# Kernel optimization log

Hardware: AMD Instinct MI355X
Metric: run time of the kernel (lower is better)

Reference implementation:

```python
import jax, jax.numpy as jnp
import numpy as np

N = 10000      # nodes
E = 320000     # edges (avg degree 32)
D_IN = 128
D_H = 256
D_C = 32       # comm_dim
D_OUT = 64


def setup_inputs() -> dict:
    key = jax.random.key(0)
    ks = jax.random.split(key, 14)
    p = lambda k, shape: jax.random.normal(k, shape, jnp.float32) * 0.02
    return {
        "x": jax.random.normal(ks[0], (N, D_IN), jnp.float32),
        "edge_index": jax.random.randint(ks[1], (2, E), 0, N),
        "W_in": p(ks[2], (D_IN, D_H)), "b_in": jnp.zeros((D_H,), jnp.float32),
        "Wq": p(ks[3], (D_H, D_C)),   "bq": jnp.zeros((D_C,), jnp.float32),
        "Wk": p(ks[4], (D_H, D_C)),   "bk": jnp.zeros((D_C,), jnp.float32),
        "Wv": p(ks[5], (D_H, D_H)),   "bv": jnp.zeros((D_H,), jnp.float32),
        "W1": p(ks[6], (2 * D_H, D_H)), "b1": jnp.zeros((D_H,), jnp.float32),
        "W2": p(ks[7], (D_H, D_OUT)),  "b2": jnp.zeros((D_OUT,), jnp.float32),
    }


def reference(x, edge_index, W_in, b_in, Wq, bq, Wk, bk, Wv, bv, W1, b1, W2, b2):
    n = x.shape[0]
    h = x @ W_in + b_in                       # [N, D_H]
    q = h @ Wq + bq                           # [N, D_C]
    k = h @ Wk + bk                           # [N, D_C]
    v = h @ Wv + bv                           # [N, D_H]
    scores = (q @ k.T) / np.sqrt(q.shape[-1]).astype(np.float32)  # [N, N]
    # torch: zeros -> scatter 1 at edges -> masked_fill(==0, -inf);
    # edge positions keep value 1.0 ADDED to scores (faithful quirk).
    mask = jnp.full((n, n), -jnp.inf, jnp.float32)
    mask = mask.at[edge_index[0], edge_index[1]].set(1.0)
    w = jax.nn.softmax(scores + mask, axis=-1)
    w = jnp.nan_to_num(w, nan=0.0)            # rows with no edges -> all zeros
    comm = w @ v                              # [N, D_H]
    combined = jnp.concatenate([h, comm], axis=-1)  # [N, 2*D_H]
    return jax.nn.relu(combined @ W1 + b1) @ W2 + b2  # [N, D_OUT]
```

## Files before the change

### kernel.cpp

```cpp
#include <hip/hip_runtime.h>
#include <stdint.h>
#include <stddef.h>

constexpr int N_NODES = 10000;
constexpr int N_EDGES = 320000;
constexpr int DIM_IN  = 128;
constexpr int DIM_H   = 256;
constexpr int DIM_C   = 32;
constexpr int DIM_OUT = 64;
constexpr int DIM_QKV = DIM_C + DIM_C + DIM_H;
constexpr int DIM_QK  = 2 * DIM_C;
constexpr int DIM_CAT = 2 * DIM_H;
constexpr float SCALE = 0.17677669529663687f;
constexpr int MAXD = 192;
constexpr float VSCALE = 64.0f;

#if __has_builtin(__builtin_amdgcn_cvt_pk_f32_fp8) && __has_builtin(__builtin_amdgcn_cvt_pk_fp8_f32)
#define V_FP8 1
#else
#define V_FP8 0
#endif

constexpr size_t alignw(size_t w) { return (w + 15) & ~size_t(15); }
constexpr size_t OFF_DEG    = 0;
constexpr size_t OFF_COL    = alignw(OFF_DEG + N_NODES);
constexpr size_t OFF_QK     = alignw(OFF_COL + (size_t)N_NODES * MAXD);
constexpr size_t OFF_BQKV   = alignw(OFF_QK + (size_t)N_NODES * DIM_QK);
constexpr size_t OFF_VBF    = alignw(OFF_BQKV + DIM_QKV);
constexpr size_t OFF_XBF    = alignw(OFF_VBF + (size_t)N_NODES * DIM_H / 2);
constexpr size_t OFF_CATBF  = alignw(OFF_XBF + (size_t)N_NODES * DIM_IN / 2);
constexpr size_t OFF_WINT   = alignw(OFF_CATBF + (size_t)N_NODES * DIM_CAT / 2);
constexpr size_t OFF_WQKVT  = alignw(OFF_WINT + (size_t)DIM_H * DIM_IN / 2);
constexpr size_t OFF_W1T    = alignw(OFF_WQKVT + (size_t)DIM_QKV * DIM_H / 2);
constexpr size_t OFF_W2T    = alignw(OFF_W1T + (size_t)DIM_H * DIM_CAT / 2);

typedef __attribute__((ext_vector_type(8))) short short8;
typedef __attribute__((ext_vector_type(4))) float floatx4;
typedef __attribute__((ext_vector_type(2))) float floatx2;

__device__ inline unsigned short f2bf(float f) {
    uint32_t u = __builtin_bit_cast(uint32_t, f);
    uint32_t r = (u + 0x7fffu + ((u >> 16) & 1u)) >> 16;
    return (unsigned short)r;
}
__device__ inline float bf2f_lo(uint32_t u) { return __builtin_bit_cast(float, u << 16); }
__device__ inline float bf2f_hi(uint32_t u) { return __builtin_bit_cast(float, u & 0xffff0000u); }

template <bool RELU, int MODE>
__global__ __launch_bounds__(256)
void mfma_gemm(const unsigned short* __restrict__ A, int lda,
               const unsigned short* __restrict__ Bt,
               const float* __restrict__ bias,
               float* __restrict__ Cf, unsigned short* __restrict__ Cb, int ldc,
               int M, int K)
{
    constexpr int BM = 128, BN = 64, PAD = 40;
    __shared__ short As[BM * PAD];
    __shared__ short Bs[BN * PAD];
    const int tid   = threadIdx.x;
    const int wave  = tid >> 6;
    const int lane  = tid & 63;
    const int quad  = lane >> 4;
    const int col16 = lane & 15;
    const int row0  = blockIdx.y * BM;
    const int col0  = blockIdx.x * BN;

    floatx4 acc[2][4] = {};

    const int sr = tid >> 2;
    const int sc = (tid & 3) * 8;

    for (int k0 = 0; k0 < K; k0 += 32) {
        #pragma unroll
        for (int i = 0; i < 2; ++i) {
            int r = sr + i * 64;
            int gr = row0 + r;
            short8 v = {};
            if (gr < M) v = *(const short8*)(A + (size_t)gr * lda + k0 + sc);
            *(short8*)(As + r * PAD + sc) = v;
        }
        {
            short8 v = *(const short8*)(Bt + (size_t)(col0 + sr) * K + k0 + sc);
            *(short8*)(Bs + sr * PAD + sc) = v;
        }
        __syncthreads();
        short8 a0 = *(const short8*)(As + (wave * 32 + col16) * PAD + quad * 8);
        short8 a1 = *(const short8*)(As + (wave * 32 + 16 + col16) * PAD + quad * 8);
        #pragma unroll
        for (int nf = 0; nf < 4; ++nf) {
            short8 b = *(const short8*)(Bs + (nf * 16 + col16) * PAD + quad * 8);
            acc[0][nf] = __builtin_amdgcn_mfma_f32_16x16x32_bf16(a0, b, acc[0][nf], 0, 0, 0);
            acc[1][nf] = __builtin_amdgcn_mfma_f32_16x16x32_bf16(a1, b, acc[1][nf], 0, 0, 0);
        }
        __syncthreads();
    }
    #pragma unroll
    for (int mf = 0; mf < 2; ++mf)
        #pragma unroll
        for (int r = 0; r < 4; ++r) {
            int gr = row0 + wave * 32 + mf * 16 + quad * 4 + r;
            if (gr >= M) continue;
            #pragma unroll
            for (int nf = 0; nf < 4; ++nf) {
                int gc = col0 + nf * 16 + col16;
                float v = acc[mf][nf][r] + bias[gc];
                if (RELU) v = fmaxf(v, 0.f);
                if (MODE == 2) {
                    if (gc < DIM_QK) {
                        Cf[(size_t)gr * DIM_QK + gc] = v;
                    } else {
#if V_FP8
                        int pk = __builtin_amdgcn_cvt_pk_fp8_f32(v * VSCALE, 0.f, 0, false);
                        ((unsigned char*)Cb)[(size_t)gr * DIM_H + (gc - DIM_QK)] =
                            (unsigned char)(pk & 0xff);
#else
                        Cb[(size_t)gr * DIM_H + (gc - DIM_QK)] = f2bf(v);
#endif
                    }
                } else {
                    Cb[(size_t)gr * ldc + gc] = f2bf(v);
                }
            }
        }
}

__global__ __launch_bounds__(256)
void gemm_w1w2(const unsigned short* __restrict__ cat, const unsigned short* __restrict__ W1T,
               const float* __restrict__ b1, const unsigned short* __restrict__ W2T,
               const float* __restrict__ b2, float* __restrict__ out, int M)
{
    constexpr int PAD = 40, TP = 260;
    __shared__ short As[64 * PAD];
    __shared__ short BsTs[64 * TP];
    short* Bs = BsTs;
    short* Ts = BsTs;
    const int tid   = threadIdx.x;
    const int wave  = tid >> 6;
    const int lane  = tid & 63;
    const int quad  = lane >> 4;
    const int col16 = lane & 15;
    const int row0  = blockIdx.x * 64;

    const int sr = tid >> 2;
    const int sc = (tid & 3) * 8;

    floatx4 acc[16] = {};
    for (int k0 = 0; k0 < DIM_CAT; k0 += 32) {
        {
            int gr = row0 + sr;
            short8 v = {};
            if (gr < M) v = *(const short8*)(cat + (size_t)gr * DIM_CAT + k0 + sc);
            *(short8*)(As + sr * PAD + sc) = v;
        }
        #pragma unroll
        for (int p = 0; p < 4; ++p) {
            int r = sr + p * 64;
            *(short8*)(Bs + r * PAD + sc) = *(const short8*)(W1T + (size_t)r * DIM_CAT + k0 + sc);
        }
        __syncthreads();
        short8 a = *(const short8*)(As + (wave * 16 + col16) * PAD + quad * 8);
        #pragma unroll
        for (int nf = 0; nf < 16; ++nf) {
            short8 b = *(const short8*)(Bs + (nf * 16 + col16) * PAD + quad * 8);
            acc[nf] = __builtin_amdgcn_mfma_f32_16x16x32_bf16(a, b, acc[nf], 0, 0, 0);
        }
        __syncthreads();
    }

    #pragma unroll
    for (int nf = 0; nf < 16; ++nf) {
        int gc = nf * 16 + col16;
        float bia = b1[gc];
        #pragma unroll
        for (int r = 0; r < 4; ++r) {
            int lr = wave * 16 + quad * 4 + r;
            float v = fmaxf(acc[nf][r] + bia, 0.f);
            Ts[lr * TP + gc] = (short)f2bf(v);
        }
    }
    __syncthreads();

    floatx4 acc2[4] = {};
    for (int k0 = 0; k0 < DIM_H; k0 += 32) {
        short8 a = *(const short8*)(Ts + (wave * 16 + col16) * TP + k0 + quad * 8);
        #pragma unroll
        for (int nf = 0; nf < 4; ++nf) {
            int brow = nf * 16 + col16;
            short8 b = *(const short8*)(W2T + (size_t)brow * DIM_H + k0 + quad * 8);
            acc2[nf] = __builtin_amdgcn_mfma_f32_16x16x32_bf16(a, b, acc2[nf], 0, 0, 0);
        }
    }
    #pragma unroll
    for (int nf = 0; nf < 4; ++nf) {
        int gc = nf * 16 + col16;
        float bia = b2[gc];
        #pragma unroll
        for (int r = 0; r < 4; ++r) {
            int gr = row0 + wave * 16 + quad * 4 + r;
            if (gr < M) out[(size_t)gr * DIM_OUT + gc] = acc2[nf][r] + bia;
        }
    }
}

__global__ void zero_deg(int* __restrict__ deg) {
    int i = blockIdx.x * blockDim.x + threadIdx.x;
    if (i < N_NODES) deg[i] = 0;
}

__global__ void prep_all(const float* __restrict__ x, const int* __restrict__ ei,
                         const float* __restrict__ W_in,
                         const float* __restrict__ Wq, const float* __restrict__ Wk,
                         const float* __restrict__ Wv,
                         const float* __restrict__ bq, const float* __restrict__ bk,
                         const float* __restrict__ bv,
                         const float* __restrict__ W1, const float* __restrict__ W2,
                         int* __restrict__ deg, int* __restrict__ col,
                         unsigned short* __restrict__ xb,
                         unsigned short* __restrict__ WinT, unsigned short* __restrict__ WqkvT,
                         unsigned short* __restrict__ W1T, unsigned short* __restrict__ W2T,
                         float* __restrict__ bqkv)
{
    int i = blockIdx.x * blockDim.x + threadIdx.x;
    int stride = gridDim.x * blockDim.x;
    for (int e = i; e < N_EDGES; e += stride) {
        int src = ei[e];
        int dst = ei[N_EDGES + e];
        int slot = atomicAdd(&deg[src], 1);
        if (slot < MAXD) col[src * MAXD + slot] = dst;
    }
    for (int idx = i; idx < (N_NODES * DIM_IN) / 8; idx += stride) {
        float4 a = ((const float4*)x)[2 * idx];
        float4 b = ((const float4*)x)[2 * idx + 1];
        uint4 o;
        o.x = (uint32_t)f2bf(a.x) | ((uint32_t)f2bf(a.y) << 16);
        o.y = (uint32_t)f2bf(a.z) | ((uint32_t)f2bf(a.w) << 16);
        o.z = (uint32_t)f2bf(b.x) | ((uint32_t)f2bf(b.y) << 16);
        o.w = (uint32_t)f2bf(b.z) | ((uint32_t)f2bf(b.w) << 16);
        ((uint4*)xb)[idx] = o;
    }
    for (int idx = i; idx < DIM_H * DIM_IN; idx += stride) {
        int n = idx / DIM_IN, k = idx % DIM_IN;
        WinT[idx] = f2bf(W_in[k * DIM_H + n]);
    }
    for (int idx = i; idx < DIM_QKV * DIM_H; idx += stride) {
        int n = idx / DIM_H, k = idx % DIM_H;
        float v = (n < DIM_C)     ? Wq[k * DIM_C + n]
                : (n < 2 * DIM_C) ? Wk[k * DIM_C + (n - DIM_C)]
                                  : Wv[k * DIM_H + (n - 2 * DIM_C)];
        WqkvT[idx] = f2bf(v);
    }
    for (int idx = i; idx < DIM_H * DIM_CAT; idx += stride) {
        int n = idx / DIM_CAT, k = idx % DIM_CAT;
        W1T[idx] = f2bf(W1[k * DIM_H + n]);
    }
    for (int idx = i; idx < DIM_OUT * DIM_H; idx += stride) {
        int n = idx / DIM_H, k = idx % DIM_H;
        W2T[idx] = f2bf(W2[k * DIM_OUT + n]);
    }
    for (int idx = i; idx < DIM_QKV; idx += stride)
        bqkv[idx] = (idx < DIM_C) ? bq[idx]
                  : (idx < 2 * DIM_C) ? bk[idx - DIM_C] : bv[idx - 2 * DIM_C];
}

__global__ __launch_bounds__(256)
void attn_row(const float* __restrict__ qk, const unsigned short* __restrict__ v_tab,
              const int* __restrict__ deg, const int* __restrict__ col,
              unsigned short* __restrict__ cat_bf) {
    __shared__ int   dstS[4][MAXD];
    __shared__ float wS[4][MAXD];
    __shared__ float qS[4][DIM_C];
    const int wave = threadIdx.x >> 6;
    const int lane = threadIdx.x & 63;
    const int row = blockIdx.x * 4 + wave;
    int d = deg[row];
    if (d > MAXD) d = MAXD;
    const int* crow = col + (size_t)row * MAXD;

    for (int p = lane; p < d; p += 64) dstS[wave][p] = crow[p];
    if (lane < DIM_C) qS[wave][lane] = qk[(size_t)row * DIM_QK + lane];
    __syncthreads();

    float mysum = 0.f;
    if (d <= 64) {
        int mydst = (lane < d) ? dstS[wave][lane] : -1;
        bool dup = false;
        #pragma unroll
        for (int k = 0; k < 63; ++k) {
            int other = __shfl(mydst, k, 64);
            dup = dup || (k < lane && other == mydst);
        }
        float w = 0.f;
        if (lane < d && !dup) {
            const float4* kp = (const float4*)(qk + (size_t)mydst * DIM_QK + DIM_C);
            float s = 0.f;
            #pragma unroll
            for (int i = 0; i < DIM_C / 4; ++i) {
                float4 b = kp[i];
                s += qS[wave][4 * i + 0] * b.x + qS[wave][4 * i + 1] * b.y
                   + qS[wave][4 * i + 2] * b.z + qS[wave][4 * i + 3] * b.w;
            }
            w = expf(s * SCALE);
        }
        wS[wave][lane] = w;
        mysum = w;
    } else {
        for (int p = lane; p < d; p += 64) {
            int mydst = dstS[wave][p];
            bool dup = false;
            for (int j = 0; j < p; ++j) dup = dup || (dstS[wave][j] == mydst);
            float w = 0.f;
            if (!dup) {
                const float4* kp = (const float4*)(qk + (size_t)mydst * DIM_QK + DIM_C);
                float s = 0.f;
                #pragma unroll
                for (int i = 0; i < DIM_C / 4; ++i) {
                    float4 b = kp[i];
                    s += qS[wave][4 * i + 0] * b.x + qS[wave][4 * i + 1] * b.y
                       + qS[wave][4 * i + 2] * b.z + qS[wave][4 * i + 3] * b.w;
                }
                w = expf(s * SCALE);
            }
            wS[wave][p] = w;
            mysum += w;
        }
    }
    #pragma unroll
    for (int off = 32; off; off >>= 1) mysum += __shfl_down(mysum, off, 64);
    float total = __shfl(mysum, 0, 64);
#if V_FP8
    float inv = (d > 0 && total > 0.f) ? 1.0f / (total * VSCALE) : 0.f;
#else
    float inv = (d > 0 && total > 0.f) ? 1.0f / total : 0.f;
#endif
    __syncthreads();

    float4 acc = make_float4(0.f, 0.f, 0.f, 0.f);
#if V_FP8
    const uint32_t* vb = (const uint32_t*)v_tab;
#else
    const uint2* vb = (const uint2*)v_tab;
#endif
    for (int p0 = 0; p0 < d; p0 += 16) {
        int j[16]; float w[16];
        #pragma unroll
        for (int t = 0; t < 16; ++t) {
            int idx = p0 + t;
            bool in = idx < d;
            j[t] = in ? dstS[wave][idx] : 0;
            w[t] = in ? wS[wave][idx] : 0.f;
        }
#if V_FP8
        uint32_t r[16];
        #pragma unroll
        for (int t = 0; t < 16; ++t) r[t] = vb[(size_t)j[t] * 64 + lane];
        #pragma unroll
        for (int t = 0; t < 16; ++t) {
            floatx2 lo = __builtin_amdgcn_cvt_pk_f32_fp8(r[t], false);
            floatx2 hi = __builtin_amdgcn_cvt_pk_f32_fp8(r[t], true);
            acc.x += w[t] * lo.x; acc.y += w[t] * lo.y;
            acc.z += w[t] * hi.x; acc.w += w[t] * hi.y;
        }
#else
        uint2 r[16];
        #pragma unroll
        for (int t = 0; t < 16; ++t) r[t] = vb[(size_t)j[t] * 64 + lane];
        #pragma unroll
        for (int t = 0; t < 16; ++t) {
            acc.x += w[t] * bf2f_lo(r[t].x);
            acc.y += w[t] * bf2f_hi(r[t].x);
            acc.z += w[t] * bf2f_lo(r[t].y);
            acc.w += w[t] * bf2f_hi(r[t].y);
        }
#endif
    }
    acc.x *= inv; acc.y *= inv; acc.z *= inv; acc.w *= inv;
    uint2 o;
    o.x = (uint32_t)f2bf(acc.x) | ((uint32_t)f2bf(acc.y) << 16);
    o.y = (uint32_t)f2bf(acc.z) | ((uint32_t)f2bf(acc.w) << 16);
    *(uint2*)(cat_bf + (size_t)row * DIM_CAT + DIM_H + lane * 4) = o;
}

extern "C" void kernel_launch(void* const* d_in, const int* in_sizes, int n_in,
                              void* d_out, int out_size, void* d_ws, size_t ws_size,
                              hipStream_t stream) {
    (void)in_sizes; (void)n_in; (void)out_size; (void)ws_size;
    const float* x    = (const float*)d_in[0];
    const int*   ei   = (const int*)d_in[1];
    const float* W_in = (const float*)d_in[2];
    const float* b_in = (const float*)d_in[3];
    const float* Wq   = (const float*)d_in[4];
    const float* bq   = (const float*)d_in[5];
    const float* Wk   = (const float*)d_in[6];
    const float* bk   = (const float*)d_in[7];
    const float* Wv   = (const float*)d_in[8];
    const float* bv   = (const float*)d_in[9];
    const float* W1   = (const float*)d_in[10];
    const float* b1   = (const float*)d_in[11];
    const float* W2   = (const float*)d_in[12];
    const float* b2   = (const float*)d_in[13];
    float* out = (float*)d_out;

    uint32_t* ws      = (uint32_t*)d_ws;
    int*      deg     = (int*)(ws + OFF_DEG);
    int*      col     = (int*)(ws + OFF_COL);
    float*    qk      = (float*)(ws + OFF_QK);
    float*    bqkv    = (float*)(ws + OFF_BQKV);
    unsigned short* v_tab  = (unsigned short*)(ws + OFF_VBF);
    unsigned short* x_bf   = (unsigned short*)(ws + OFF_XBF);
    unsigned short* cat_bf = (unsigned short*)(ws + OFF_CATBF);
    unsigned short* WinT   = (unsigned short*)(ws + OFF_WINT);
    unsigned short* WqkvT  = (unsigned short*)(ws + OFF_WQKVT);
    unsigned short* W1T    = (unsigned short*)(ws + OFF_W1T);
    unsigned short* W2T    = (unsigned short*)(ws + OFF_W2T);

    zero_deg<<<(N_NODES + 255) / 256, 256, 0, stream>>>(deg);
    prep_all<<<640, 256, 0, stream>>>(x, ei, W_in, Wq, Wk, Wv, bq, bk, bv, W1, W2,
                                      deg, col, x_bf, WinT, WqkvT, W1T, W2T, bqkv);

    const int MB = (N_NODES + 127) / 128;
    mfma_gemm<false, 1><<<dim3(DIM_H / 64, MB), 256, 0, stream>>>(
        x_bf, DIM_IN, WinT, b_in, nullptr, cat_bf, DIM_CAT, N_NODES, DIM_IN);
    mfma_gemm<false, 2><<<dim3(DIM_QKV / 64, MB), 256, 0, stream>>>(
        cat_bf, DIM_CAT, WqkvT, bqkv, qk, v_tab, 0, N_NODES, DIM_H);
    attn_row<<<N_NODES / 4, 256, 0, stream>>>(qk, v_tab, deg, col, cat_bf);
    gemm_w1w2<<<(N_NODES + 63) / 64, 256, 0, stream>>>(
        cat_bf, W1T, b1, W2T, b2, out, N_NODES);
}
```

Baseline: 177.9 us.

## Fuse all stages into one persistent kernel with global atomic barriers

Replaces the six separate launches (zero, prep, two GEMMs, attention, MLP) with a single persistent kernel of 256 blocks that runs each stage in turn and separates stages with software grid barriers built on atomic counters. The GEMM tiles also change to larger per-wave register blocking (4x4 and 4x5 MFMA fragments). The aim is to remove launch gaps and tail effects between small kernels. In exchange, stages that are sized for fewer blocks leave some blocks idle, and the spin barriers rely on all 256 blocks being co-resident on the device.

```diff
diff --git a/kernel.cpp b/kernel.cpp
--- a/kernel.cpp
+++ b/kernel.cpp
@@ -15,6 +15,10 @@
 constexpr int MAXD = 192;
 constexpr float VSCALE = 64.0f;
 
+constexpr int NBLK = 256;
+constexpr int NTHR = 256;
+constexpr int PAD  = 40;
+
 #if __has_builtin(__builtin_amdgcn_cvt_pk_f32_fp8) && __has_builtin(__builtin_amdgcn_cvt_pk_fp8_f32)
 #define V_FP8 1
 #else
@@ -22,21 +26,24 @@
 #endif
 
 constexpr size_t alignw(size_t w) { return (w + 15) & ~size_t(15); }
-constexpr size_t OFF_DEG    = 0;
-constexpr size_t OFF_COL    = alignw(OFF_DEG + N_NODES);
-constexpr size_t OFF_QK     = alignw(OFF_COL + (size_t)N_NODES * MAXD);
-constexpr size_t OFF_BQKV   = alignw(OFF_QK + (size_t)N_NODES * DIM_QK);
-constexpr size_t OFF_VBF    = alignw(OFF_BQKV + DIM_QKV);
-constexpr size_t OFF_XBF    = alignw(OFF_VBF + (size_t)N_NODES * DIM_H / 2);
-constexpr size_t OFF_CATBF  = alignw(OFF_XBF + (size_t)N_NODES * DIM_IN / 2);
-constexpr size_t OFF_WINT   = alignw(OFF_CATBF + (size_t)N_NODES * DIM_CAT / 2);
-constexpr size_t OFF_WQKVT  = alignw(OFF_WINT + (size_t)DIM_H * DIM_IN / 2);
-constexpr size_t OFF_W1T    = alignw(OFF_WQKVT + (size_t)DIM_QKV * DIM_H / 2);
-constexpr size_t OFF_W2T    = alignw(OFF_W1T + (size_t)DIM_H * DIM_CAT / 2);
+constexpr size_t OFF_DEG   = 0;
+constexpr size_t OFF_BAR   = OFF_DEG + N_NODES;
+constexpr size_t OFF_COL   = alignw(OFF_BAR + 16);
+constexpr size_t OFF_QK    = alignw(OFF_COL + (size_t)N_NODES * MAXD);
+constexpr size_t OFF_BQKV  = alignw(OFF_QK + (size_t)N_NODES * DIM_QK);
+constexpr size_t OFF_VT    = alignw(OFF_BQKV + DIM_QKV);
+constexpr size_t OFF_XBF   = alignw(OFF_VT + (size_t)N_NODES * DIM_H / 2);
+constexpr size_t OFF_CATBF = alignw(OFF_XBF + (size_t)N_NODES * DIM_IN / 2);
+constexpr size_t OFF_WINT  = alignw(OFF_CATBF + (size_t)N_NODES * DIM_CAT / 2);
+constexpr size_t OFF_WQKVT = alignw(OFF_WINT + (size_t)DIM_H * DIM_IN / 2);
+constexpr size_t OFF_W1T   = alignw(OFF_WQKVT + (size_t)DIM_QKV * DIM_H / 2);
+constexpr size_t OFF_W2T   = alignw(OFF_W1T + (size_t)DIM_H * DIM_CAT / 2);
 
 typedef __attribute__((ext_vector_type(8))) short short8;
 typedef __attribute__((ext_vector_type(4))) float floatx4;
 typedef __attribute__((ext_vector_type(2))) float floatx2;
+
+#define MFMA16 __builtin_amdgcn_mfma_f32_16x16x32_bf16
 
 __device__ inline unsigned short f2bf(float f) {
     uint32_t u = __builtin_bit_cast(uint32_t, f);
@@ -46,338 +53,394 @@
 __device__ inline float bf2f_lo(uint32_t u) { return __builtin_bit_cast(float, u << 16); }
 __device__ inline float bf2f_hi(uint32_t u) { return __builtin_bit_cast(float, u & 0xffff0000u); }
 
-template <bool RELU, int MODE>
-__global__ __launch_bounds__(256)
-void mfma_gemm(const unsigned short* __restrict__ A, int lda,
-               const unsigned short* __restrict__ Bt,
-               const float* __restrict__ bias,
-               float* __restrict__ Cf, unsigned short* __restrict__ Cb, int ldc,
-               int M, int K)
+__device__ inline void gbar(int* bar, int idx) {
+    __syncthreads();
+    if (threadIdx.x == 0) {
+        __threadfence();
+        __hip_atomic_fetch_add(&bar[idx], 1, __ATOMIC_RELEASE, __HIP_MEMORY_SCOPE_AGENT);
+        while (__hip_atomic_load(&bar[idx], __ATOMIC_ACQUIRE, __HIP_MEMORY_SCOPE_AGENT) < NBLK)
+            __builtin_amdgcn_s_sleep(2);
+        __threadfence();
+    }
+    __syncthreads();
+}
+
+__global__ __launch_bounds__(NTHR)
+void mega(const float* __restrict__ x, const int* __restrict__ ei,
+          const float* __restrict__ W_in, const float* __restrict__ b_in,
+          const float* __restrict__ Wq, const float* __restrict__ bq,
+          const float* __restrict__ Wk, const float* __restrict__ bk,
+          const float* __restrict__ Wv, const float* __restrict__ bv,
+          const float* __restrict__ W1, const float* __restrict__ b1,
+          const float* __restrict__ W2, const float* __restrict__ b2,
+          float* __restrict__ out,
+          int* __restrict__ deg, int* __restrict__ bar, int* __restrict__ col,
+          float* __restrict__ qk, float* __restrict__ bqkv,
+          unsigned short* __restrict__ v_tab, unsigned short* __restrict__ x_bf,
+          unsigned short* __restrict__ cat_bf,
+          unsigned short* __restrict__ WinT, unsigned short* __restrict__ WqkvT,
+          unsigned short* __restrict__ W1T, unsigned short* __restrict__ W2T)
 {
-    constexpr int BM = 128, BN = 64, PAD = 40;
-    __shared__ short As[BM * PAD];
-    __shared__ short Bs[BN * PAD];
+    __shared__ alignas(16) char SMEM[38400];
     const int tid   = threadIdx.x;
+    const int bid   = blockIdx.x;
     const int wave  = tid >> 6;
     const int lane  = tid & 63;
     const int quad  = lane >> 4;
     const int col16 = lane & 15;
-    const int row0  = blockIdx.y * BM;
-    const int col0  = blockIdx.x * BN;
-
-    floatx4 acc[2][4] = {};
-
-    const int sr = tid >> 2;
-    const int sc = (tid & 3) * 8;
-
-    for (int k0 = 0; k0 < K; k0 += 32) {
-        #pragma unroll
-        for (int i = 0; i < 2; ++i) {
-            int r = sr + i * 64;
-            int gr = row0 + r;
-            short8 v = {};
-            if (gr < M) v = *(const short8*)(A + (size_t)gr * lda + k0 + sc);
-            *(short8*)(As + r * PAD + sc) = v;
-        }
-        {
-            short8 v = *(const short8*)(Bt + (size_t)(col0 + sr) * K + k0 + sc);
-            *(short8*)(Bs + sr * PAD + sc) = v;
-        }
-        __syncthreads();
-        short8 a0 = *(const short8*)(As + (wave * 32 + col16) * PAD + quad * 8);
-        short8 a1 = *(const short8*)(As + (wave * 32 + 16 + col16) * PAD + quad * 8);
-        #pragma unroll
-        for (int nf = 0; nf < 4; ++nf) {
-            short8 b = *(const short8*)(Bs + (nf * 16 + col16) * PAD + quad * 8);
-            acc[0][nf] = __builtin_amdgcn_mfma_f32_16x16x32_bf16(a0, b, acc[0][nf], 0, 0, 0);
-            acc[1][nf] = __builtin_amdgcn_mfma_f32_16x16x32_bf16(a1, b, acc[1][nf], 0, 0, 0);
-        }
-        __syncthreads();
-    }
-    #pragma unroll
-    for (int mf = 0; mf < 2; ++mf)
-        #pragma unroll
-        for (int r = 0; r < 4; ++r) {
-            int gr = row0 + wave * 32 + mf * 16 + quad * 4 + r;
-            if (gr >= M) continue;
+    const int sr    = tid >> 2;
+    const int sc    = (tid & 3) * 8;
+
+    {
+        const int i0 = bid * NTHR + tid;
+        const int stride = NBLK * NTHR;
+        for (int e = i0; e < N_EDGES; e += stride) {
+            int src = ei[e];
+            int dst = ei[N_EDGES + e];
+            int slot = atomicAdd(&deg[src], 1);
+            if (slot < MAXD) col[src * MAXD + slot] = dst;
+        }
+        for (int idx = i0; idx < (N_NODES * DIM_IN) / 8; idx += stride) {
+            float4 a = ((const float4*)x)[2 * idx];
+            float4 b = ((const float4*)x)[2 * idx + 1];
+            uint4 o;
+            o.x = (uint32_t)f2bf(a.x) | ((uint32_t)f2bf(a.y) << 16);
+            o.y = (uint32_t)f2bf(a.z) | ((uint32_t)f2bf(a.w) << 16);
+            o.z = (uint32_t)f2bf(b.x) | ((uint32_t)f2bf(b.y) << 16);
+            o.w = (uint32_t)f2bf(b.z) | ((uint32_t)f2bf(b.w) << 16);
+            ((uint4*)x_bf)[idx] = o;
+        }
+        for (int idx = i0; idx < DIM_H * DIM_IN; idx += stride) {
+            int n = idx / DIM_IN, k = idx % DIM_IN;
+            WinT[idx] = f2bf(W_in[k * DIM_H + n]);
+        }
+        for (int idx = i0; idx < DIM_QKV * DIM_H; idx += stride) {
+            int n = idx / DIM_H, k = idx % DIM_H;
+            float v = (n < DIM_C)     ? Wq[k * DIM_C + n]
+                    : (n < 2 * DIM_C) ? Wk[k * DIM_C + (n - DIM_C)]
+                                      : Wv[k * DIM_H + (n - 2 * DIM_C)];
+            WqkvT[idx] = f2bf(v);
+        }
+        for (int idx = i0; idx < DIM_H * DIM_CAT; idx += stride) {
+            int n = idx / DIM_CAT, k = idx % DIM_CAT;
+            W1T[idx] = f2bf(W1[k * DIM_H + n]);
+        }
+        for (int idx = i0; idx < DIM_OUT * DIM_H; idx += stride) {
+            int n = idx / DIM_H, k = idx % DIM_H;
+            W2T[idx] = f2bf(W2[k * DIM_OUT + n]);
+        }
+        for (int idx = i0; idx < DIM_QKV; idx += stride)
+            bqkv[idx] = (idx < DIM_C) ? bq[idx]
+                      : (idx < 2 * DIM_C) ? bk[idx - DIM_C] : bv[idx - 2 * DIM_C];
+    }
+    gbar(bar, 0);
+
+    {
+        short* As = (short*)SMEM;
+        short* Bs = (short*)(SMEM + 10240);
+        if (bid < 2 * ((N_NODES + 127) / 128)) {
+            const int row0 = (bid >> 1) * 128;
+            const int col0 = (bid & 1) * 128;
+            const int wr = wave >> 1, wc = wave & 1;
+            floatx4 acc[4][4] = {};
+            for (int k0 = 0; k0 < DIM_IN; k0 += 32) {
+                #pragma unroll
+                for (int i2 = 0; i2 < 2; ++i2) {
+                    int r = sr + i2 * 64, gr = row0 + r;
+                    short8 v = {};
+                    if (gr < N_NODES) v = *(const short8*)(x_bf + (size_t)gr * DIM_IN + k0 + sc);
+                    *(short8*)(As + r * PAD + sc) = v;
+                }
+                #pragma unroll
+                for (int i2 = 0; i2 < 2; ++i2) {
+                    int r = sr + i2 * 64;
+                    *(short8*)(Bs + r * PAD + sc) =
+                        *(const short8*)(WinT + (size_t)(col0 + r) * DIM_IN + k0 + sc);
+                }
+                __syncthreads();
+                short8 af[4], bf[4];
+                #pragma unroll
+                for (int m = 0; m < 4; ++m)
+                    af[m] = *(const short8*)(As + (wr * 64 + m * 16 + col16) * PAD + quad * 8);
+                #pragma unroll
+                for (int n = 0; n < 4; ++n)
+                    bf[n] = *(const short8*)(Bs + (wc * 64 + n * 16 + col16) * PAD + quad * 8);
+                #pragma unroll
+                for (int m = 0; m < 4; ++m)
+                    #pragma unroll
+                    for (int n = 0; n < 4; ++n)
+                        acc[m][n] = MFMA16(af[m], bf[n], acc[m][n], 0, 0, 0);
+                __syncthreads();
+            }
             #pragma unroll
-            for (int nf = 0; nf < 4; ++nf) {
-                int gc = col0 + nf * 16 + col16;
-                float v = acc[mf][nf][r] + bias[gc];
-                if (RELU) v = fmaxf(v, 0.f);
-                if (MODE == 2) {
-                    if (gc < DIM_QK) {
-                        Cf[(size_t)gr * DIM_QK + gc] = v;
-                    } else {
+            for (int m = 0; m < 4; ++m)
+                #pragma unroll
+                for (int n = 0; n < 4; ++n) {
+                    int gc = col0 + wc * 64 + n * 16 + col16;
+                    float bia = b_in[gc];
+                    #pragma unroll
+                    for (int r = 0; r < 4; ++r) {
+                        int gr = row0 + wr * 64 + m * 16 + quad * 4 + r;
+                        if (gr < N_NODES)
+                            cat_bf[(size_t)gr * DIM_CAT + gc] = f2bf(acc[m][n][r] + bia);
+                    }
+                }
+        }
+    }
+    gbar(bar, 1);
+
+    {
+        short* As = (short*)SMEM;
+        short* Bs = (short*)(SMEM + 10240);
+        if (bid < 2 * ((N_NODES + 127) / 128)) {
+            const int row0 = (bid >> 1) * 128;
+            const int col0 = (bid & 1) * 160;
+            const int wr = wave >> 1, wc = wave & 1;
+            floatx4 acc[4][5] = {};
+            for (int k0 = 0; k0 < DIM_H; k0 += 32) {
+                #pragma unroll
+                for (int i2 = 0; i2 < 2; ++i2) {
+                    int r = sr + i2 * 64, gr = row0 + r;
+                    short8 v = {};
+                    if (gr < N_NODES) v = *(const short8*)(cat_bf + (size_t)gr * DIM_CAT + k0 + sc);
+                    *(short8*)(As + r * PAD + sc) = v;
+                }
+                #pragma unroll
+                for (int i2 = 0; i2 < 3; ++i2) {
+                    int r = sr + i2 * 64;
+                    if (r < 160)
+                        *(short8*)(Bs + r * PAD + sc) =
+                            *(const short8*)(WqkvT + (size_t)(col0 + r) * DIM_H + k0 + sc);
+                }
+                __syncthreads();
+                short8 af[4], bf[5];
+                #pragma unroll
+                for (int m = 0; m < 4; ++m)
+                    af[m] = *(const short8*)(As + (wr * 64 + m * 16 + col16) * PAD + quad * 8);
+                #pragma unroll
+                for (int n = 0; n < 5; ++n)
+                    bf[n] = *(const short8*)(Bs + (wc * 80 + n * 16 + col16) * PAD + quad * 8);
+                #pragma unroll
+                for (int m = 0; m < 4; ++m)
+                    #pragma unroll
+                    for (int n = 0; n < 5; ++n)
+                        acc[m][n] = MFMA16(af[m], bf[n], acc[m][n], 0, 0, 0);
+                __syncthreads();
+            }
+            #pragma unroll
+            for (int m = 0; m < 4; ++m)
+                #pragma unroll
+                for (int n = 0; n < 5; ++n) {
+                    int gc = col0 + wc * 80 + n * 16 + col16;
+                    float bia = bqkv[gc];
+                    #pragma unroll
+                    for (int r = 0; r < 4; ++r) {
+                        int gr = row0 + wr * 64 + m * 16 + quad * 4 + r;
+                        if (gr >= N_NODES) continue;
+                        float v = acc[m][n][r] + bia;
+                        if (gc < DIM_QK) {
+                            qk[(size_t)gr * DIM_QK + gc] = v;
+                        } else {
 #if V_FP8
-                        int pk = __builtin_amdgcn_cvt_pk_fp8_f32(v * VSCALE, 0.f, 0, false);
-                        ((unsigned char*)Cb)[(size_t)gr * DIM_H + (gc - DIM_QK)] =
-                            (unsigned char)(pk & 0xff);
+                            int pk = __builtin_amdgcn_cvt_pk_fp8_f32(v * VSCALE, 0.f, 0, false);
+                            ((unsigned char*)v_tab)[(size_t)gr * DIM_H + (gc - DIM_QK)] =
+                                (unsigned char)(pk & 0xff);
 #else
-                        Cb[(size_t)gr * DIM_H + (gc - DIM_QK)] = f2bf(v);
+                            v_tab[(size_t)gr * DIM_H + (gc - DIM_QK)] = f2bf(v);
 #endif
+                        }
                     }
-                } else {
-                    Cb[(size_t)gr * ldc + gc] = f2bf(v);
-                }
-            }
-        }
-}
-
-__global__ __launch_bounds__(256)
-void gemm_w1w2(const unsigned short* __restrict__ cat, const unsigned short* __restrict__ W1T,
-               const float* __restrict__ b1, const unsigned short* __restrict__ W2T,
-               const float* __restrict__ b2, float* __restrict__ out, int M)
-{
-    constexpr int PAD = 40, TP = 260;
-    __shared__ short As[64 * PAD];
-    __shared__ short BsTs[64 * TP];
-    short* Bs = BsTs;
-    short* Ts = BsTs;
-    const int tid   = threadIdx.x;
-    const int wave  = tid >> 6;
-    const int lane  = tid & 63;
-    const int quad  = lane >> 4;
-    const int col16 = lane & 15;
-    const int row0  = blockIdx.x * 64;
-
-    const int sr = tid >> 2;
-    const int sc = (tid & 3) * 8;
-
-    floatx4 acc[16] = {};
-    for (int k0 = 0; k0 < DIM_CAT; k0 += 32) {
-        {
-            int gr = row0 + sr;
-            short8 v = {};
-            if (gr < M) v = *(const short8*)(cat + (size_t)gr * DIM_CAT + k0 + sc);
-            *(short8*)(As + sr * PAD + sc) = v;
-        }
-        #pragma unroll
-        for (int p = 0; p < 4; ++p) {
-            int r = sr + p * 64;
-            *(short8*)(Bs + r * PAD + sc) = *(const short8*)(W1T + (size_t)r * DIM_CAT + k0 + sc);
-        }
-        __syncthreads();
-        short8 a = *(const short8*)(As + (wave * 16 + col16) * PAD + quad * 8);
-        #pragma unroll
-        for (int nf = 0; nf < 16; ++nf) {
-            short8 b = *(const short8*)(Bs + (nf * 16 + col16) * PAD + quad * 8);
-            acc[nf] = __builtin_amdgcn_mfma_f32_16x16x32_bf16(a, b, acc[nf], 0, 0, 0);
-        }
-        __syncthreads();
-    }
-
-    #pragma unroll
-    for (int nf = 0; nf < 16; ++nf) {
-        int gc = nf * 16 + col16;
-        float bia = b1[gc];
-        #pragma unroll
-        for (int r = 0; r < 4; ++r) {
-            int lr = wave * 16 + quad * 4 + r;
-            float v = fmaxf(acc[nf][r] + bia, 0.f);
-            Ts[lr * TP + gc] = (short)f2bf(v);
-        }
-    }
-    __syncthreads();
-
-    floatx4 acc2[4] = {};
-    for (int k0 = 0; k0 < DIM_H; k0 += 32) {
-        short8 a = *(const short8*)(Ts + (wave * 16 + col16) * TP + k0 + quad * 8);
-        #pragma unroll
-        for (int nf = 0; nf < 4; ++nf) {
-            int brow = nf * 16 + col16;
-            short8 b = *(const short8*)(W2T + (size_t)brow * DIM_H + k0 + quad * 8);
-            acc2[nf] = __builtin_amdgcn_mfma_f32_16x16x32_bf16(a, b, acc2[nf], 0, 0, 0);
-        }
-    }
-    #pragma unroll
-    for (int nf = 0; nf < 4; ++nf) {
-        int gc = nf * 16 + col16;
-        float bia = b2[gc];
-        #pragma unroll
-        for (int r = 0; r < 4; ++r) {
-            int gr = row0 + wave * 16 + quad * 4 + r;
-            if (gr < M) out[(size_t)gr * DIM_OUT + gc] = acc2[nf][r] + bia;
-        }
-    }
-}
-
-__global__ void zero_deg(int* __restrict__ deg) {
-    int i = blockIdx.x * blockDim.x + threadIdx.x;
-    if (i < N_NODES) deg[i] = 0;
-}
-
-__global__ void prep_all(const float* __restrict__ x, const int* __restrict__ ei,
-                         const float* __restrict__ W_in,
-                         const float* __restrict__ Wq, const float* __restrict__ Wk,
-                         const float* __restrict__ Wv,
-                         const float* __restrict__ bq, const float* __restrict__ bk,
-                         const float* __restrict__ bv,
-                         const float* __restrict__ W1, const float* __restrict__ W2,
-                         int* __restrict__ deg, int* __restrict__ col,
-                         unsigned short* __restrict__ xb,
-                         unsigned short* __restrict__ WinT, unsigned short* __restrict__ WqkvT,
-                         unsigned short* __restrict__ W1T, unsigned short* __restrict__ W2T,
-                         float* __restrict__ bqkv)
-{
-    int i = blockIdx.x * blockDim.x + threadIdx.x;
-    int stride = gridDim.x * blockDim.x;
-    for (int e = i; e < N_EDGES; e += stride) {
-        int src = ei[e];
-        int dst = ei[N_EDGES + e];
-        int slot = atomicAdd(&deg[src], 1);
-        if (slot < MAXD) col[src * MAXD + slot] = dst;
-    }
-    for (int idx = i; idx < (N_NODES * DIM_IN) / 8; idx += stride) {
-        float4 a = ((const float4*)x)[2 * idx];
-        float4 b = ((const float4*)x)[2 * idx + 1];
-        uint4 o;
-        o.x = (uint32_t)f2bf(a.x) | ((uint32_t)f2bf(a.y) << 16);
-        o.y = (uint32_t)f2bf(a.z) | ((uint32_t)f2bf(a.w) << 16);
-        o.z = (uint32_t)f2bf(b.x) | ((uint32_t)f2bf(b.y) << 16);
-        o.w = (uint32_t)f2bf(b.z) | ((uint32_t)f2bf(b.w) << 16);
-        ((uint4*)xb)[idx] = o;
-    }
-    for (int idx = i; idx < DIM_H * DIM_IN; idx += stride) {
-        int n = idx / DIM_IN, k = idx % DIM_IN;
-        WinT[idx] = f2bf(W_in[k * DIM_H + n]);
-    }
-    for (int idx = i; idx < DIM_QKV * DIM_H; idx += stride) {
-        int n = idx / DIM_H, k = idx % DIM_H;
-        float v = (n < DIM_C)     ? Wq[k * DIM_C + n]
-                : (n < 2 * DIM_C) ? Wk[k * DIM_C + (n - DIM_C)]
-                                  : Wv[k * DIM_H + (n - 2 * DIM_C)];
-        WqkvT[idx] = f2bf(v);
-    }
-    for (int idx = i; idx < DIM_H * DIM_CAT; idx += stride) {
-        int n = idx / DIM_CAT, k = idx % DIM_CAT;
-        W1T[idx] = f2bf(W1[k * DIM_H + n]);
-    }
-    for (int idx = i; idx < DIM_OUT * DIM_H; idx += stride) {
-        int n = idx / DIM_H, k = idx % DIM_H;
-        W2T[idx] = f2bf(W2[k * DIM_OUT + n]);
-    }
-    for (int idx = i; idx < DIM_QKV; idx += stride)
-        bqkv[idx] = (idx < DIM_C) ? bq[idx]
-                  : (idx < 2 * DIM_C) ? bk[idx - DIM_C] : bv[idx - 2 * DIM_C];
-}
-
-__global__ __launch_bounds__(256)
-void attn_row(const float* __restrict__ qk, const unsigned short* __restrict__ v_tab,
-              const int* __restrict__ deg, const int* __restrict__ col,
-              unsigned short* __restrict__ cat_bf) {
-    __shared__ int   dstS[4][MAXD];
-    __shared__ float wS[4][MAXD];
-    __shared__ float qS[4][DIM_C];
-    const int wave = threadIdx.x >> 6;
-    const int lane = threadIdx.x & 63;
-    const int row = blockIdx.x * 4 + wave;
-    int d = deg[row];
-    if (d > MAXD) d = MAXD;
-    const int* crow = col + (size_t)row * MAXD;
-
-    for (int p = lane; p < d; p += 64) dstS[wave][p] = crow[p];
-    if (lane < DIM_C) qS[wave][lane] = qk[(size_t)row * DIM_QK + lane];
-    __syncthreads();
-
-    float mysum = 0.f;
-    if (d <= 64) {
-        int mydst = (lane < d) ? dstS[wave][lane] : -1;
-        bool dup = false;
-        #pragma unroll
-        for (int k = 0; k < 63; ++k) {
-            int other = __shfl(mydst, k, 64);
-            dup = dup || (k < lane && other == mydst);
-        }
-        float w = 0.f;
-        if (lane < d && !dup) {
-            const float4* kp = (const float4*)(qk + (size_t)mydst * DIM_QK + DIM_C);
-            float s = 0.f;
+                }
+        }
+    }
+    gbar(bar, 2);
+
+    {
+        int*   dstW = (int*)SMEM + wave * MAXD;
+        float* wW   = (float*)(SMEM + 3072) + wave * MAXD;
+        float* qW   = (float*)(SMEM + 6144) + wave * DIM_C;
+        for (int row = bid * 4 + wave; row < N_NODES; row += NBLK * 4) {
+            __threadfence_block();
+            int d = deg[row];
+            if (d > MAXD) d = MAXD;
+            const int* crow = col + (size_t)row * MAXD;
+
+            for (int p = lane; p < d; p += 64) dstW[p] = crow[p];
+            if (lane < DIM_C) qW[lane] = qk[(size_t)row * DIM_QK + lane];
+            __threadfence_block();
+
+            float mysum = 0.f;
+            if (d <= 64) {
+                int mydst = (lane < d) ? dstW[lane] : -1;
+                bool dup = false;
+                for (int k2 = 0; k2 < d - 1; ++k2) {
+                    int other = __shfl(mydst, k2, 64);
+                    dup = dup || (k2 < lane && other == mydst);
+                }
+                float w = 0.f;
+                if (lane < d && !dup) {
+                    const float4* kp = (const float4*)(qk + (size_t)mydst * DIM_QK + DIM_C);
+                    float s = 0.f;
+                    #pragma unroll
+                    for (int i = 0; i < DIM_C / 4; ++i) {
+                        float4 b = kp[i];
+                        s += qW[4 * i + 0] * b.x + qW[4 * i + 1] * b.y
+                           + qW[4 * i + 2] * b.z + qW[4 * i + 3] * b.w;
+                    }
+                    w = expf(s * SCALE);
+                }
+                wW[lane] = w;
+                mysum = w;
+            } else {
+                for (int p = lane; p < d; p += 64) {
+                    int mydst = dstW[p];
+                    bool dup = false;
+                    for (int j = 0; j < p; ++j) dup = dup || (dstW[j] == mydst);
+                    float w = 0.f;
+                    if (!dup) {
+                        const float4* kp = (const float4*)(qk + (size_t)mydst * DIM_QK + DIM_C);
+                        float s = 0.f;
+                        #pragma unroll
+                        for (int i = 0; i < DIM_C / 4; ++i) {
+                            float4 b = kp[i];
+                            s += qW[4 * i + 0] * b.x + qW[4 * i + 1] * b.y
+                               + qW[4 * i + 2] * b.z + qW[4 * i + 3] * b.w;
+                        }
+                        w = expf(s * SCALE);
+                    }
+                    wW[p] = w;
+                    mysum += w;
+                }
+            }
             #pragma unroll
-            for (int i = 0; i < DIM_C / 4; ++i) {
-                float4 b = kp[i];
-                s += qS[wave][4 * i + 0] * b.x + qS[wave][4 * i + 1] * b.y
-                   + qS[wave][4 * i + 2] * b.z + qS[wave][4 * i + 3] * b.w;
-            }
-            w = expf(s * SCALE);
-        }
-        wS[wave][lane] = w;
-        mysum = w;
-    } else {
-        for (int p = lane; p < d; p += 64) {
-            int mydst = dstS[wave][p];
-            bool dup = false;
-            for (int j = 0; j < p; ++j) dup = dup || (dstS[wave][j] == mydst);
-            float w = 0.f;
-            if (!dup) {
-                const float4* kp = (const float4*)(qk + (size_t)mydst * DIM_QK + DIM_C);
-                float s = 0.f;
-                #pragma unroll
-                for (int i = 0; i < DIM_C / 4; ++i) {
-                    float4 b = kp[i];
-                    s += qS[wave][4 * i + 0] * b.x + qS[wave][4 * i + 1] * b.y
-                       + qS[wave][4 * i + 2] * b.z + qS[wave][4 * i + 3] * b.w;
-                }
-                w = expf(s * SCALE);
-            }
-            wS[wave][p] = w;
-            mysum += w;
-        }
-    }
-    #pragma unroll
-    for (int off = 32; off; off >>= 1) mysum += __shfl_down(mysum, off, 64);
-    float total = __shfl(mysum, 0, 64);
+            for (int off = 32; off; off >>= 1) mysum += __shfl_down(mysum, off, 64);
+            float total = __shfl(mysum, 0, 64);
 #if V_FP8
-    float inv = (d > 0 && total > 0.f) ? 1.0f / (total * VSCALE) : 0.f;
+            float inv = (d > 0 && total > 0.f) ? 1.0f / (total * VSCALE) : 0.f;
 #else
-    float inv = (d > 0 && total > 0.f) ? 1.0f / total : 0.f;
+            float inv = (d > 0 && total > 0.f) ? 1.0f / total : 0.f;
 #endif
-    __syncthreads();
-
-    float4 acc = make_float4(0.f, 0.f, 0.f, 0.f);
+            __threadfence_block();
+
+            float4 acc = make_float4(0.f, 0.f, 0.f, 0.f);
 #if V_FP8
-    const uint32_t* vb = (const uint32_t*)v_tab;
+            const uint32_t* vb = (const uint32_t*)v_tab;
 #else
-    const uint2* vb = (const uint2*)v_tab;
+            const uint2* vb = (const uint2*)v_tab;
 #endif
-    for (int p0 = 0; p0 < d; p0 += 16) {
-        int j[16]; float w[16];
-        #pragma unroll
-        for (int t = 0; t < 16; ++t) {
-            int idx = p0 + t;
-            bool in = idx < d;
-            j[t] = in ? dstS[wave][idx] : 0;
-            w[t] = in ? wS[wave][idx] : 0.f;
-        }
+            for (int p0 = 0; p0 < d; p0 += 16) {
+                int j[16]; float w[16];
+                #pragma unroll
+                for (int t = 0; t < 16; ++t) {
+                    int idx = p0 + t;
+                    bool in = idx < d;
+                    j[t] = in ? dstW[idx] : 0;
+                    w[t] = in ? wW[idx] : 0.f;
+                }
 #if V_FP8
-        uint32_t r[16];
-        #pragma unroll
-        for (int t = 0; t < 16; ++t) r[t] = vb[(size_t)j[t] * 64 + lane];
-        #pragma unroll
-        for (int t = 0; t < 16; ++t) {
-            floatx2 lo = __builtin_amdgcn_cvt_pk_f32_fp8(r[t], false);
-            floatx2 hi = __builtin_amdgcn_cvt_pk_f32_fp8(r[t], true);
-            acc.x += w[t] * lo.x; acc.y += w[t] * lo.y;
-            acc.z += w[t] * hi.x; acc.w += w[t] * hi.y;
-        }
+                uint32_t r[16];
+                #pragma unroll
+                for (int t = 0; t < 16; ++t) r[t] = vb[(size_t)j[t] * 64 + lane];
+                #pragma unroll
+                for (int t = 0; t < 16; ++t) {
+                    floatx2 lo = __builtin_amdgcn_cvt_pk_f32_fp8(r[t], false);
+                    floatx2 hi = __builtin_amdgcn_cvt_pk_f32_fp8(r[t], true);
+                    acc.x += w[t] * lo.x; acc.y += w[t] * lo.y;
+                    acc.z += w[t] * hi.x; acc.w += w[t] * hi.y;
+                }
 #else
-        uint2 r[16];
-        #pragma unroll
-        for (int t = 0; t < 16; ++t) r[t] = vb[(size_t)j[t] * 64 + lane];
-        #pragma unroll
-        for (int t = 0; t < 16; ++t) {
-            acc.x += w[t] * bf2f_lo(r[t].x);
-            acc.y += w[t] * bf2f_hi(r[t].x);
-            acc.z += w[t] * bf2f_lo(r[t].y);
-            acc.w += w[t] * bf2f_hi(r[t].y);
-        }
+                uint2 r[16];
+                #pragma unroll
+                for (int t = 0; t < 16; ++t) r[t] = vb[(size_t)j[t] * 64 + lane];
+                #pragma unroll
+                for (int t = 0; t < 16; ++t) {
+                    acc.x += w[t] * bf2f_lo(r[t].x);
+                    acc.y += w[t] * bf2f_hi(r[t].x);
+                    acc.z += w[t] * bf2f_lo(r[t].y);
+                    acc.w += w[t] * bf2f_hi(r[t].y);
+                }
 #endif
-    }
-    acc.x *= inv; acc.y *= inv; acc.z *= inv; acc.w *= inv;
-    uint2 o;
-    o.x = (uint32_t)f2bf(acc.x) | ((uint32_t)f2bf(acc.y) << 16);
-    o.y = (uint32_t)f2bf(acc.z) | ((uint32_t)f2bf(acc.w) << 16);
-    *(uint2*)(cat_bf + (size_t)row * DIM_CAT + DIM_H + lane * 4) = o;
+            }
+            acc.x *= inv; acc.y *= inv; acc.z *= inv; acc.w *= inv;
+            uint2 o;
+            o.x = (uint32_t)f2bf(acc.x) | ((uint32_t)f2bf(acc.y) << 16);
+            o.y = (uint32_t)f2bf(acc.z) | ((uint32_t)f2bf(acc.w) << 16);
+            *(uint2*)(cat_bf + (size_t)row * DIM_CAT + DIM_H + lane * 4) = o;
+        }
+    }
+    gbar(bar, 3);
+
+    {
+        constexpr int TP = 260;
+        short* As   = (short*)SMEM;
+        short* BsTs = (short*)(SMEM + 5120);
+        short* Bs = BsTs;
+        short* Ts = BsTs;
+        if (bid < (N_NODES + 63) / 64) {
+            const int row0 = bid * 64;
+            floatx4 acc[4][4] = {};
+            for (int k0 = 0; k0 < DIM_CAT; k0 += 32) {
+                {
+                    int gr = row0 + sr;
+                    short8 v = {};
+                    if (gr < N_NODES) v = *(const short8*)(cat_bf + (size_t)gr * DIM_CAT + k0 + sc);
+                    *(short8*)(As + sr * PAD + sc) = v;
+                }
+                #pragma unroll
+                for (int p = 0; p < 4; ++p) {
+                    int r = sr + p * 64;
+                    *(short8*)(Bs + r * PAD + sc) =
+                        *(const short8*)(W1T + (size_t)r * DIM_CAT + k0 + sc);
+                }
+                __syncthreads();
+                short8 af[4], bf[4];
+                #pragma unroll
+                for (int m = 0; m < 4; ++m)
+                    af[m] = *(const short8*)(As + (m * 16 + col16) * PAD + quad * 8);
+                #pragma unroll
+                for (int n = 0; n < 4; ++n)
+                    bf[n] = *(const short8*)(Bs + (wave * 64 + n * 16 + col16) * PAD + quad * 8);
+                #pragma unroll
+                for (int m = 0; m < 4; ++m)
+                    #pragma unroll
+                    for (int n = 0; n < 4; ++n)
+                        acc[m][n] = MFMA16(af[m], bf[n], acc[m][n], 0, 0, 0);
+                __syncthreads();
+            }
+            #pragma unroll
+            for (int m = 0; m < 4; ++m)
+                #pragma unroll
+                for (int n = 0; n < 4; ++n) {
+                    int gc = wave * 64 + n * 16 + col16;
+                    float bia = b1[gc];
+                    #pragma unroll
+                    for (int r = 0; r < 4; ++r) {
+                        int lr = m * 16 + quad * 4 + r;
+                        Ts[lr * TP + gc] = (short)f2bf(fmaxf(acc[m][n][r] + bia, 0.f));
+                    }
+                }
+            __syncthreads();
+            floatx4 acc2[4] = {};
+            for (int k0 = 0; k0 < DIM_H; k0 += 32) {
+                short8 a = *(const short8*)(Ts + (wave * 16 + col16) * TP + k0 + quad * 8);
+                #pragma unroll
+                for (int n = 0; n < 4; ++n) {
+                    short8 b = *(const short8*)(W2T + (size_t)(n * 16 + col16) * DIM_H + k0 + quad * 8);
+                    acc2[n] = MFMA16(a, b, acc2[n], 0, 0, 0);
+                }
+            }
+            #pragma unroll
+            for (int n = 0; n < 4; ++n) {
+                int gc = n * 16 + col16;
+                float bia = b2[gc];
+                #pragma unroll
+                for (int r = 0; r < 4; ++r) {
+                    int gr = row0 + wave * 16 + quad * 4 + r;
+                    if (gr < N_NODES) out[(size_t)gr * DIM_OUT + gc] = acc2[n][r] + bia;
+                }
+            }
+        }
+    }
 }
 
 extern "C" void kernel_launch(void* const* d_in, const int* in_sizes, int n_in,
@@ -402,10 +465,11 @@
 
     uint32_t* ws      = (uint32_t*)d_ws;
     int*      deg     = (int*)(ws + OFF_DEG);
+    int*      bar     = (int*)(ws + OFF_BAR);
     int*      col     = (int*)(ws + OFF_COL);
     float*    qk      = (float*)(ws + OFF_QK);
     float*    bqkv    = (float*)(ws + OFF_BQKV);
-    unsigned short* v_tab  = (unsigned short*)(ws + OFF_VBF);
+    unsigned short* v_tab  = (unsigned short*)(ws + OFF_VT);
     unsigned short* x_bf   = (unsigned short*)(ws + OFF_XBF);
     unsigned short* cat_bf = (unsigned short*)(ws + OFF_CATBF);
     unsigned short* WinT   = (unsigned short*)(ws + OFF_WINT);
@@ -413,16 +477,9 @@
     unsigned short* W1T    = (unsigned short*)(ws + OFF_W1T);
     unsigned short* W2T    = (unsigned short*)(ws + OFF_W2T);
 
-    zero_deg<<<(N_NODES + 255) / 256, 256, 0, stream>>>(deg);
-    prep_all<<<640, 256, 0, stream>>>(x, ei, W_in, Wq, Wk, Wv, bq, bk, bv, W1, W2,
-                                      deg, col, x_bf, WinT, WqkvT, W1T, W2T, bqkv);
-
-    const int MB = (N_NODES + 127) / 128;
-    mfma_gemm<false, 1><<<dim3(DIM_H / 64, MB), 256, 0, stream>>>(
-        x_bf, DIM_IN, WinT, b_in, nullptr, cat_bf, DIM_CAT, N_NODES, DIM_IN);
-    mfma_gemm<false, 2><<<dim3(DIM_QKV / 64, MB), 256, 0, stream>>>(
-        cat_bf, DIM_CAT, WqkvT, bqkv, qk, v_tab, 0, N_NODES, DIM_H);
-    attn_row<<<N_NODES / 4, 256, 0, stream>>>(qk, v_tab, deg, col, cat_bf);
-    gemm_w1w2<<<(N_NODES + 63) / 64, 256, 0, stream>>>(
-        cat_bf, W1T, b1, W2T, b2, out, N_NODES);
+    hipMemsetAsync(ws, 0, (OFF_BAR + 16) * sizeof(uint32_t), stream);
+    hipLaunchKernelGGL(mega, dim3(NBLK), dim3(NTHR), 0, stream,
+                       x, ei, W_in, b_in, Wq, bq, Wk, bk, Wv, bv, W1, b1, W2, b2, out,
+                       deg, bar, col, qk, bqkv, v_tab, x_bf, cat_bf,
+                       WinT, WqkvT, W1T, W2T);
 }
```

New measurement: 421.6 us. 137% more time.
